# Performance work log

Hardware: AMD Instinct MI355X
Metric: run time of the kernel (lower is better)

Reference implementation:

```python
import jax, jax.numpy as jnp
import numpy as np

HID = 16

def _lrconv(x, edge_index, edge_attr, w1, b1, w2, b2):
    # flow='target_to_source': x_i = x[edge_index[0]], x_j = x[edge_index[1]],
    # aggregate (max) at edge_index[0].
    src = edge_index[0]
    dst = edge_index[1]
    m = jnp.concatenate([x[src], x[dst], edge_attr], axis=-1)  # [E, 2*in+edge]
    m = jax.nn.relu(m @ w1 + b1)
    m = jax.nn.relu(m @ w2 + b2)  # [E, out], all >= 0
    agg = jax.ops.segment_max(m, src, num_segments=x.shape[0])
    # empty segments get -inf in jax; PyG fills with 0. Messages are ReLU'd (>=0),
    # so clamping at 0 is exact.
    return jnp.maximum(agg, 0.0)

def _glorot(key, shape):
    fan_in, fan_out = shape
    lim = float(np.sqrt(6.0 / (fan_in + fan_out)))
    return jax.random.uniform(key, shape, jnp.float32, -lim, lim)

def setup_inputs() -> dict:
    key = jax.random.key(0)
    ks = jax.random.split(key, 16)
    N, E = 100000, 1600000
    x = jax.random.normal(ks[0], (N, 4), jnp.float32)
    edge_index = jax.random.randint(ks[1], (2, E), 0, N, jnp.int64)
    edge_attr = jax.random.normal(ks[2], (E, 8), jnp.float32)
    # conv1: in=4 -> cat dim 4*2+8=16
    c1_w1 = _glorot(ks[3], (16, HID)); c1_b1 = jnp.zeros((HID,), jnp.float32)
    c1_w2 = _glorot(ks[4], (HID, 16)); c1_b2 = jnp.zeros((16,), jnp.float32)
    # conv2: in=16 -> cat dim 16*2+8=40
    c2_w1 = _glorot(ks[5], (40, HID)); c2_b1 = jnp.zeros((HID,), jnp.float32)
    c2_w2 = _glorot(ks[6], (HID, 16)); c2_b2 = jnp.zeros((16,), jnp.float32)
    l1_w = _glorot(ks[7], (16, 16)); l1_b = jnp.zeros((16,), jnp.float32)
    l2_w = _glorot(ks[8], (16, 1)); l2_b = jnp.zeros((1,), jnp.float32)
    return {"x": x, "edge_index": edge_index, "edge_attr": edge_attr,
            "c1_w1": c1_w1, "c1_b1": c1_b1, "c1_w2": c1_w2, "c1_b2": c1_b2,
            "c2_w1": c2_w1, "c2_b1": c2_b1, "c2_w2": c2_w2, "c2_b2": c2_b2,
            "l1_w": l1_w, "l1_b": l1_b, "l2_w": l2_w, "l2_b": l2_b}

def reference(x, edge_index, edge_attr,
              c1_w1, c1_b1, c1_w2, c1_b2,
              c2_w1, c2_b1, c2_w2, c2_b2,
              l1_w, l1_b, l2_w, l2_b):
    h = _lrconv(x, edge_index, edge_attr, c1_w1, c1_b1, c1_w2, c1_b2)   # [N,16]
    h = _lrconv(h, edge_index, edge_attr, c2_w1, c2_b1, c2_w2, c2_b2)   # [N,16]
    h = jax.nn.relu(h @ l1_w + l1_b)
    return h @ l2_w + l2_b  # [N,1]
```

## Files before the change

### kernel.cpp

```cpp
#include <hip/hip_runtime.h>
#include <hip/hip_fp16.h>

#define CHUNK 1024
#define RECB 24
#define SPAN 192

typedef _Float16 half8 __attribute__((ext_vector_type(8)));
typedef _Float16 half4 __attribute__((ext_vector_type(4)));
typedef float floatx4 __attribute__((ext_vector_type(4)));

__device__ __forceinline__ unsigned int pack2f(float a, float b) {
    __half2 h = __floats2half2_rn(a, b);
    return *(unsigned int*)&h;
}

__device__ __forceinline__ half8 load_attr(const char* __restrict__ rec, int et) {
    union { unsigned int u[4]; half8 h; } cv;
    uint2 lo = *(const uint2*)(rec + (size_t)et * RECB + 8);
    uint2 hi = *(const uint2*)(rec + (size_t)et * RECB + 16);
    cv.u[0] = lo.x; cv.u[1] = lo.y; cv.u[2] = hi.x; cv.u[3] = hi.y;
    return cv.h;
}

__global__ __launch_bounds__(256) void rank_cvt(
    const int* __restrict__ ei, const float* __restrict__ x,
    int* __restrict__ deg, unsigned short* __restrict__ r,
    _Float16* __restrict__ xh, int E, int N)
{
    int e = blockIdx.x * 256 + threadIdx.x;
    if (e >= E) return;
    r[e] = (unsigned short)atomicAdd(&deg[ei[e]], 1);
    if (e < N) {
        float4 xv = *(const float4*)(x + (size_t)e * 4);
        half4 hx;
        hx[0] = (_Float16)xv.x; hx[1] = (_Float16)xv.y;
        hx[2] = (_Float16)xv.z; hx[3] = (_Float16)xv.w;
        *(half4*)(xh + (size_t)e * 4) = hx;
    }
}

__global__ __launch_bounds__(256) void scan_chunk_sums(
    const int* __restrict__ v, int* __restrict__ csum, int N)
{
    __shared__ int s[256];
    int base = blockIdx.x * CHUNK;
    int t = threadIdx.x;
    int acc = 0;
    #pragma unroll
    for (int i = 0; i < CHUNK / 256; ++i) {
        int idx = base + t + i * 256;
        if (idx < N) acc += v[idx];
    }
    s[t] = acc; __syncthreads();
    for (int o = 128; o > 0; o >>= 1) {
        if (t < o) s[t] += s[t + o];
        __syncthreads();
    }
    if (t == 0) csum[blockIdx.x] = s[0];
}

__global__ __launch_bounds__(256) void scan_chunk_off(
    const int* __restrict__ csum, int* __restrict__ coff, int nch)
{
    __shared__ int s[256];
    __shared__ int carry;
    int t = threadIdx.x;
    if (t == 0) carry = 0;
    __syncthreads();
    for (int base = 0; base < nch; base += 256) {
        int v = (base + t < nch) ? csum[base + t] : 0;
        s[t] = v; __syncthreads();
        for (int o = 1; o < 256; o <<= 1) {
            int add = (t >= o) ? s[t - o] : 0;
            __syncthreads();
            s[t] += add;
            __syncthreads();
        }
        int excl = carry + (t > 0 ? s[t - 1] : 0);
        if (base + t < nch) coff[base + t] = excl;
        __syncthreads();
        if (t == 0) carry += s[255];
        __syncthreads();
    }
}

__global__ __launch_bounds__(256) void scan_within_excl(
    const int* __restrict__ deg, int* __restrict__ pos,
    const int* __restrict__ coff, int N)
{
    __shared__ int s[256];
    int t = threadIdx.x;
    int base = blockIdx.x * CHUNK + t * 4;
    int v0 = 0, v1 = 0, v2 = 0, v3 = 0;
    if (base + 0 < N) v0 = deg[base + 0];
    if (base + 1 < N) v1 = deg[base + 1];
    if (base + 2 < N) v2 = deg[base + 2];
    if (base + 3 < N) v3 = deg[base + 3];
    s[t] = v0 + v1 + v2 + v3;
    __syncthreads();
    for (int o = 1; o < 256; o <<= 1) {
        int add = (t >= o) ? s[t - o] : 0;
        __syncthreads();
        s[t] += add;
        __syncthreads();
    }
    int run = coff[blockIdx.x] + (t > 0 ? s[t - 1] : 0);
    if (base + 0 < N) pos[base + 0] = run; run += v0;
    if (base + 1 < N) pos[base + 1] = run; run += v1;
    if (base + 2 < N) pos[base + 2] = run; run += v2;
    if (base + 3 < N) pos[base + 3] = run;
}

__global__ __launch_bounds__(256) void scatter_rec(
    const int* __restrict__ ei, const float* __restrict__ ea,
    const int* __restrict__ pos, const unsigned short* __restrict__ r,
    char* __restrict__ rec, int E)
{
    int e = blockIdx.x * 256 + threadIdx.x;
    if (e >= E) return;
    int s = ei[e];
    int d = ei[E + e];
    int p = pos[s] + (int)r[e];
    float4 a0 = *(const float4*)(ea + (size_t)e * 8);
    float4 a1 = *(const float4*)(ea + (size_t)e * 8 + 4);
    unsigned int h0 = pack2f(a0.x, a0.y), h1 = pack2f(a0.z, a0.w);
    unsigned int h2 = pack2f(a1.x, a1.y), h3 = pack2f(a1.z, a1.w);
    char* b = rec + (size_t)p * RECB;
    *(int2*)b         = make_int2(s, d);
    *(uint2*)(b + 8)  = make_uint2(h0, h1);
    *(uint2*)(b + 16) = make_uint2(h2, h3);
}

__global__ __launch_bounds__(256) void edge_mlp1_agg(
    const _Float16* __restrict__ xh,
    const char*  __restrict__ rec,
    const float* __restrict__ w1, const float* __restrict__ b1,
    const float* __restrict__ w2, const float* __restrict__ b2,
    int* __restrict__ aggi,
    int E)
{
    __shared__ _Float16 itm[4][8][16][24];
    __shared__ int lmax[SPAN * 16];
    int tid = threadIdx.x;
    int w = tid >> 6, lane = tid & 63;
    int e16 = lane & 15, q = lane >> 4;
    int kb = blockIdx.x * 512;
    int ebase = kb + (w << 7);
    int e0 = ebase + lane;
    int e1 = ebase + 64 + lane;

    #pragma unroll
    for (int i = 0; i < SPAN * 16 / 256; ++i) lmax[tid + i * 256] = 0;

    int klast = min(kb + 511, E - 1);
    int n_first = *(const int*)(rec + (size_t)kb * RECB);
    int n_last  = *(const int*)(rec + (size_t)klast * RECB);
    int span = n_last - n_first + 1;
    bool fb = (span > SPAN);
    __syncthreads();

    int s0 = 0, d0 = 0, s1 = 0, d1 = 0;
    if (e0 < E) { int2 p = *(const int2*)(rec + (size_t)e0 * RECB); s0 = p.x; d0 = p.y; }
    if (e1 < E) { int2 p = *(const int2*)(rec + (size_t)e1 * RECB); s1 = p.x; d1 = p.y; }

    half8 B1, B2;
    #pragma unroll
    for (int j = 0; j < 8; ++j) { B1[j] = (_Float16)0.f; B2[j] = (_Float16)0.f; }
    if (q < 2) {
        #pragma unroll
        for (int j = 0; j < 8; ++j) {
            B1[j] = (_Float16)w1[(8 * q + j) * 16 + e16];
            B2[j] = (_Float16)w2[(8 * q + j) * 16 + e16];
        }
    }
    float b1c = b1[e16], b2c = b2[e16];

    half8 A[8];
    #pragma unroll
    for (int t = 0; t < 8; ++t) {
        int tt = t & 3;
        int st = (t < 4) ? __shfl(s0, 16 * tt + e16, 64) : __shfl(s1, 16 * tt + e16, 64);
        int dt = (t < 4) ? __shfl(d0, 16 * tt + e16, 64) : __shfl(d1, 16 * tt + e16, 64);
        half8 a;
        #pragma unroll
        for (int j = 0; j < 8; ++j) a[j] = (_Float16)0.f;
        int et = ebase + 16 * t + e16;
        if (q == 0 && et < E) {
            half4 hs = *(const half4*)(xh + (size_t)st * 4);
            half4 hd = *(const half4*)(xh + (size_t)dt * 4);
            a[0] = hs[0]; a[1] = hs[1]; a[2] = hs[2]; a[3] = hs[3];
            a[4] = hd[0]; a[5] = hd[1]; a[6] = hd[2]; a[7] = hd[3];
        } else if (q == 1 && et < E) {
            a = load_attr(rec, et);
        }
        A[t] = a;
    }

    floatx4 C[8];
    #pragma unroll
    for (int t = 0; t < 8; ++t) {
        floatx4 c = {b1c, b1c, b1c, b1c};
        C[t] = __builtin_amdgcn_mfma_f32_16x16x32_f16(A[t], B1, c, 0, 0, 0);
    }
    #pragma unroll
    for (int t = 0; t < 8; ++t)
        #pragma unroll
        for (int i = 0; i < 4; ++i)
            itm[w][t][4 * q + i][e16] = (_Float16)fmaxf(C[t][i], 0.0f);
    __builtin_amdgcn_wave_barrier();

    half8 A2[8];
    #pragma unroll
    for (int t = 0; t < 8; ++t) {
        half8 a;
        #pragma unroll
        for (int j = 0; j < 8; ++j) a[j] = (_Float16)0.f;
        if (q < 2) a = *(const half8*)&itm[w][t][e16][8 * q];
        A2[t] = a;
    }
    __builtin_amdgcn_wave_barrier();
    floatx4 C2[8];
    #pragma unroll
    for (int t = 0; t < 8; ++t) {
        floatx4 c = {b2c, b2c, b2c, b2c};
        C2[t] = __builtin_amdgcn_mfma_f32_16x16x32_f16(A2[t], B2, c, 0, 0, 0);
    }

    #pragma unroll
    for (int t = 0; t < 8; ++t) {
        int tt = t & 3;
        #pragma unroll
        for (int i = 0; i < 4; ++i) {
            int rr = 4 * q + i;
            int nn = (t < 4) ? __shfl(s0, 16 * tt + rr, 64) : __shfl(s1, 16 * tt + rr, 64);
            int et = ebase + 16 * t + rr;
            if (et < E) {
                int bits = __float_as_int(fmaxf(C2[t][i], 0.0f));
                if (!fb) atomicMax(&lmax[(nn - n_first) * 16 + e16], bits);
                else     atomicMax(&aggi[(size_t)nn * 16 + e16], bits);
            }
        }
    }
    __syncthreads();
    if (!fb) {
        int tot = span * 16;
        for (int idx = tid; idx < tot; idx += 256) {
            int row = idx >> 4;
            int nn = n_first + row;
            int v = lmax[idx];
            if (nn == n_first || nn == n_last) {
                if (v != 0) atomicMax(&aggi[(size_t)nn * 16 + (idx & 15)], v);
            } else {
                aggi[(size_t)nn * 16 + (idx & 15)] = v;
            }
        }
    }
}

__global__ __launch_bounds__(256) void cvt_h1(
    const int* __restrict__ aggi, unsigned int* __restrict__ h1u, int total)
{
    int i = blockIdx.x * 256 + threadIdx.x;
    if (i >= total) return;
    int2 v = *(const int2*)(aggi + 2 * i);
    h1u[i] = pack2f(__int_as_float(v.x), __int_as_float(v.y));
}

__global__ __launch_bounds__(256) void edge_mlp2_agg(
    const _Float16* __restrict__ h1,
    const char*  __restrict__ rec,
    const float* __restrict__ w1, const float* __restrict__ b1v,
    const float* __restrict__ w2, const float* __restrict__ b2,
    int* __restrict__ aggi, int E)
{
    __shared__ _Float16 itm[4][8][16][24];
    __shared__ int lmax[SPAN * 16];
    int tid = threadIdx.x;
    int w = tid >> 6, lane = tid & 63;
    int e16 = lane & 15, q = lane >> 4;
    int kb = blockIdx.x * 512;
    int ebase = kb + (w << 7);
    int e0 = ebase + lane;
    int e1 = ebase + 64 + lane;

    #pragma unroll
    for (int i = 0; i < SPAN * 16 / 256; ++i) lmax[tid + i * 256] = 0;

    int klast = min(kb + 511, E - 1);
    int n_first = *(const int*)(rec + (size_t)kb * RECB);
    int n_last  = *(const int*)(rec + (size_t)klast * RECB);
    int span = n_last - n_first + 1;
    bool fb = (span > SPAN);
    __syncthreads();

    int s0 = 0, d0 = 0, s1 = 0, d1 = 0;
    if (e0 < E) { int2 p = *(const int2*)(rec + (size_t)e0 * RECB); s0 = p.x; d0 = p.y; }
    if (e1 < E) { int2 p = *(const int2*)(rec + (size_t)e1 * RECB); s1 = p.x; d1 = p.y; }

    half8 B1, B2e, BL2;
    #pragma unroll
    for (int j = 0; j < 8; ++j) {
        B1[j] = (_Float16)w1[(8 * q + j) * 16 + e16];
        B2e[j] = (_Float16)0.f; BL2[j] = (_Float16)0.f;
    }
    if (q == 0) {
        #pragma unroll
        for (int j = 0; j < 8; ++j)
            B2e[j] = (_Float16)w1[(32 + j) * 16 + e16];
    }
    if (q < 2) {
        #pragma unroll
        for (int j = 0; j < 8; ++j)
            BL2[j] = (_Float16)w2[(8 * q + j) * 16 + e16];
    }
    float b1c = b1v[e16], b2c = b2[e16];

    half8 A1[8];
    #pragma unroll
    for (int t = 0; t < 8; ++t) {
        int tt = t & 3;
        int st = (t < 4) ? __shfl(s0, 16 * tt + e16, 64) : __shfl(s1, 16 * tt + e16, 64);
        int dt = (t < 4) ? __shfl(d0, 16 * tt + e16, 64) : __shfl(d1, 16 * tt + e16, 64);
        int row = (q < 2) ? st : dt;
        A1[t] = *(const half8*)(h1 + (size_t)row * 16 + 8 * (q & 1));
    }

    floatx4 C[8];
    #pragma unroll
    for (int t = 0; t < 8; ++t) {
        half8 a2;
        #pragma unroll
        for (int j = 0; j < 8; ++j) a2[j] = (_Float16)0.f;
        int et = ebase + 16 * t + e16;
        if (q == 0 && et < E)
            a2 = load_attr(rec, et);
        floatx4 c = {b1c, b1c, b1c, b1c};
        c = __builtin_amdgcn_mfma_f32_16x16x32_f16(a2, B2e, c, 0, 0, 0);
        C[t] = __builtin_amdgcn_mfma_f32_16x16x32_f16(A1[t], B1, c, 0, 0, 0);
    }
    #pragma unroll
    for (int t = 0; t < 8; ++t)
        #pragma unroll
        for (int i = 0; i < 4; ++i)
            itm[w][t][4 * q + i][e16] = (_Float16)fmaxf(C[t][i], 0.0f);
    __builtin_amdgcn_wave_barrier();

    half8 A2L[8];
    #pragma unroll
    for (int t = 0; t < 8; ++t) {
        half8 a;
        #pragma unroll
        for (int j = 0; j < 8; ++j) a[j] = (_Float16)0.f;
        if (q < 2) a = *(const half8*)&itm[w][t][e16][8 * q];
        A2L[t] = a;
    }
    __builtin_amdgcn_wave_barrier();
    floatx4 C2[8];
    #pragma unroll
    for (int t = 0; t < 8; ++t) {
        floatx4 c = {b2c, b2c, b2c, b2c};
        C2[t] = __builtin_amdgcn_mfma_f32_16x16x32_f16(A2L[t], BL2, c, 0, 0, 0);
    }

    #pragma unroll
    for (int t = 0; t < 8; ++t) {
        int tt = t & 3;
        #pragma unroll
        for (int i = 0; i < 4; ++i) {
            int rr = 4 * q + i;
            int nn = (t < 4) ? __shfl(s0, 16 * tt + rr, 64) : __shfl(s1, 16 * tt + rr, 64);
            int et = ebase + 16 * t + rr;
            if (et < E) {
                int bits = __float_as_int(fmaxf(C2[t][i], 0.0f));
                if (!fb) atomicMax(&lmax[(nn - n_first) * 16 + e16], bits);
                else     atomicMax(&aggi[(size_t)nn * 16 + e16], bits);
            }
        }
    }
    __syncthreads();
    if (!fb) {
        int tot = span * 16;
        for (int idx = tid; idx < tot; idx += 256) {
            int row = idx >> 4;
            int nn = n_first + row;
            int v = lmax[idx];
            if (nn == n_first || nn == n_last) {
                if (v != 0) atomicMax(&aggi[(size_t)nn * 16 + (idx & 15)], v);
            } else {
                aggi[(size_t)nn * 16 + (idx & 15)] = v;
            }
        }
    }
}

__global__ __launch_bounds__(256) void head_out(
    const int* __restrict__ aggi,
    const float* __restrict__ l1w, const float* __restrict__ l1b,
    const float* __restrict__ l2w, const float* __restrict__ l2b,
    float* __restrict__ out, int N)
{
    int n = blockIdx.x * 256 + threadIdx.x;
    if (n >= N) return;
    const float4* ar = (const float4*)(aggi + (size_t)n * 16);
    float4 A0 = ar[0], A1 = ar[1], A2 = ar[2], A3 = ar[3];
    float acc[16] = {A0.x, A0.y, A0.z, A0.w, A1.x, A1.y, A1.z, A1.w,
                     A2.x, A2.y, A2.z, A2.w, A3.x, A3.y, A3.z, A3.w};
    float t2[16];
    #pragma unroll
    for (int j = 0; j < 16; ++j) t2[j] = l1b[j];
    #pragma unroll
    for (int k = 0; k < 16; ++k) {
        float ak = acc[k];
        #pragma unroll
        for (int j = 0; j < 16; ++j) t2[j] = fmaf(ak, l1w[k * 16 + j], t2[j]);
    }
    float r2 = l2b[0];
    #pragma unroll
    for (int j = 0; j < 16; ++j) r2 = fmaf(fmaxf(t2[j], 0.0f), l2w[j], r2);
    out[n] = r2;
}

extern "C" void kernel_launch(void* const* d_in, const int* in_sizes, int n_in,
                              void* d_out, int out_size, void* d_ws, size_t ws_size,
                              hipStream_t stream)
{
    const float* x     = (const float*)d_in[0];
    const int*   ei    = (const int*)  d_in[1];
    const float* ea    = (const float*)d_in[2];
    const float* c1_w1 = (const float*)d_in[3];
    const float* c1_b1 = (const float*)d_in[4];
    const float* c1_w2 = (const float*)d_in[5];
    const float* c1_b2 = (const float*)d_in[6];
    const float* c2_w1 = (const float*)d_in[7];
    const float* c2_b1 = (const float*)d_in[8];
    const float* c2_w2 = (const float*)d_in[9];
    const float* c2_b2 = (const float*)d_in[10];
    const float* l1_w  = (const float*)d_in[11];
    const float* l1_b  = (const float*)d_in[12];
    const float* l2_w  = (const float*)d_in[13];
    const float* l2_b  = (const float*)d_in[14];
    float* out = (float*)d_out;

    const int N = in_sizes[0] / 4;
    const int E = in_sizes[2] / 8;
    const int nch = (N + CHUNK - 1) / CHUNK;

    const int BLK = 256;
    const int egrid = (E + BLK - 1) / BLK;
    const int mgrid = (E + 511) / 512;
    const int ngrid = (N + 255) / 256;
    const int cgrid = (N * 8 + 255) / 256;

    size_t szPos = ((size_t)N * 4 + 255) & ~(size_t)255;
    size_t szR   = ((size_t)E * 2 + 255) & ~(size_t)255;
    size_t szXh  = ((size_t)N * 8 + 255) & ~(size_t)255;
    size_t szH1  = ((size_t)N * 32 + 255) & ~(size_t)255;
    size_t szRec = ((size_t)E * RECB + 255) & ~(size_t)255;
    size_t szAgg = ((size_t)N * 16 * 4 + 255) & ~(size_t)255;
    size_t szDeg = szPos;

    size_t pos_off  = 0;
    size_t r_off    = pos_off  + szPos;
    size_t xh_off   = r_off    + szR;
    size_t h1_off   = xh_off   + szXh;
    size_t rec_off  = h1_off   + szH1;
    size_t agg1_off = rec_off  + szRec;
    size_t agg2_off = agg1_off + szAgg;
    size_t deg_off  = agg2_off + szAgg;
    size_t cs_off   = deg_off  + szDeg;
    size_t cf_off   = cs_off   + 4096;

    int*            pos  = (int*)  ((char*)d_ws + pos_off);
    unsigned short* r    = (unsigned short*)((char*)d_ws + r_off);
    _Float16*       xh   = (_Float16*)((char*)d_ws + xh_off);
    _Float16*       h1   = (_Float16*)((char*)d_ws + h1_off);
    char*           rec  = (char*) ((char*)d_ws + rec_off);
    int*            agg1 = (int*)  ((char*)d_ws + agg1_off);
    int*            agg2 = (int*)  ((char*)d_ws + agg2_off);
    int*            deg  = (int*)  ((char*)d_ws + deg_off);
    int*            csum = (int*)  ((char*)d_ws + cs_off);
    int*            coff = (int*)  ((char*)d_ws + cf_off);

    hipMemsetAsync(deg, 0, (size_t)N * 4, stream);
    hipMemsetAsync(agg1, 0, (size_t)N * 64, stream);
    hipMemsetAsync(agg2, 0, (size_t)N * 64, stream);
    rank_cvt<<<egrid, BLK, 0, stream>>>(ei, x, deg, r, xh, E, N);
    scan_chunk_sums<<<nch, BLK, 0, stream>>>(deg, csum, N);
    scan_chunk_off<<<1, 256, 0, stream>>>(csum, coff, nch);
    scan_within_excl<<<nch, BLK, 0, stream>>>(deg, pos, coff, N);
    scatter_rec<<<egrid, BLK, 0, stream>>>(ei, ea, pos, r, rec, E);
    edge_mlp1_agg<<<mgrid, BLK, 0, stream>>>(xh, rec,
                                             c1_w1, c1_b1, c1_w2, c1_b2,
                                             agg1, E);
    cvt_h1<<<cgrid, BLK, 0, stream>>>(agg1, (unsigned int*)h1, N * 8);
    edge_mlp2_agg<<<mgrid, BLK, 0, stream>>>(h1, rec,
                                             c2_w1, c2_b1, c2_w2, c2_b2,
                                             agg2, E);
    head_out<<<ngrid, BLK, 0, stream>>>(agg2, l1_w, l1_b, l2_w, l2_b, out, N);
}
```

Baseline: 324.9 us.

## Replace global-atomic counting sort with two-pass bucketed partition into split SoA arrays

The per-edge global atomic rank plus random 24-byte record scatter is replaced by a two-level counting sort. Per-block shared-memory histograms over 512-node buckets are scanned, edges are partitioned into buckets, then each bucket is sorted by source in shared memory. Records are split into an int2 src/dst array and a 16-byte attribute array, so the MLP kernels use aligned vector loads. This trades global atomic contention and scattered writes for an extra full pass over the edge data, and reuses the partition buffers for the aggregation arrays.

```diff
diff --git a/kernel.cpp b/kernel.cpp
--- a/kernel.cpp
+++ b/kernel.cpp
@@ -2,7 +2,8 @@
 #include <hip/hip_fp16.h>
 
 #define CHUNK 1024
-#define RECB 24
+#define NBLK 256
+#define NSH  9
 #define SPAN 192
 
 typedef _Float16 half8 __attribute__((ext_vector_type(8)));
@@ -14,29 +15,35 @@
     return *(unsigned int*)&h;
 }
 
-__device__ __forceinline__ half8 load_attr(const char* __restrict__ rec, int et) {
-    union { unsigned int u[4]; half8 h; } cv;
-    uint2 lo = *(const uint2*)(rec + (size_t)et * RECB + 8);
-    uint2 hi = *(const uint2*)(rec + (size_t)et * RECB + 16);
-    cv.u[0] = lo.x; cv.u[1] = lo.y; cv.u[2] = hi.x; cv.u[3] = hi.y;
+__device__ __forceinline__ half8 load_attr(const uint4* __restrict__ rat, int et) {
+    union { uint4 u; half8 h; } cv;
+    cv.u = rat[et];
     return cv.h;
 }
 
-__global__ __launch_bounds__(256) void rank_cvt(
+__global__ __launch_bounds__(512) void hist_x(
     const int* __restrict__ ei, const float* __restrict__ x,
-    int* __restrict__ deg, unsigned short* __restrict__ r,
-    _Float16* __restrict__ xh, int E, int N)
-{
-    int e = blockIdx.x * 256 + threadIdx.x;
-    if (e >= E) return;
-    r[e] = (unsigned short)atomicAdd(&deg[ei[e]], 1);
-    if (e < N) {
-        float4 xv = *(const float4*)(x + (size_t)e * 4);
-        half4 hx;
-        hx[0] = (_Float16)xv.x; hx[1] = (_Float16)xv.y;
-        hx[2] = (_Float16)xv.z; hx[3] = (_Float16)xv.w;
-        *(half4*)(xh + (size_t)e * 4) = hx;
-    }
+    int* __restrict__ cnt, _Float16* __restrict__ xh,
+    int E, int N, int nbk, int epb)
+{
+    __shared__ int h[256];
+    int t = threadIdx.x, b = blockIdx.x;
+    if (t < 256) h[t] = 0;
+    __syncthreads();
+    int est = b * epb;
+    int een = min(E, est + epb);
+    for (int e = est + t; e < een; e += 512)
+        atomicAdd(&h[ei[e] >> NSH], 1);
+    for (int i = est + t; i < een; i += 512)
+        if (i < N) {
+            float4 xv = *(const float4*)(x + (size_t)i * 4);
+            half4 hx;
+            hx[0] = (_Float16)xv.x; hx[1] = (_Float16)xv.y;
+            hx[2] = (_Float16)xv.z; hx[3] = (_Float16)xv.w;
+            *(half4*)(xh + (size_t)i * 4) = hx;
+        }
+    __syncthreads();
+    if (t < nbk) cnt[t * NBLK + b] = h[t];
 }
 
 __global__ __launch_bounds__(256) void scan_chunk_sums(
@@ -111,29 +118,69 @@
     if (base + 3 < N) pos[base + 3] = run;
 }
 
-__global__ __launch_bounds__(256) void scatter_rec(
+__global__ __launch_bounds__(512) void partition(
     const int* __restrict__ ei, const float* __restrict__ ea,
-    const int* __restrict__ pos, const unsigned short* __restrict__ r,
-    char* __restrict__ rec, int E)
-{
-    int e = blockIdx.x * 256 + threadIdx.x;
-    if (e >= E) return;
-    int s = ei[e];
-    int d = ei[E + e];
-    int p = pos[s] + (int)r[e];
-    float4 a0 = *(const float4*)(ea + (size_t)e * 8);
-    float4 a1 = *(const float4*)(ea + (size_t)e * 8 + 4);
-    unsigned int h0 = pack2f(a0.x, a0.y), h1 = pack2f(a0.z, a0.w);
-    unsigned int h2 = pack2f(a1.x, a1.y), h3 = pack2f(a1.z, a1.w);
-    char* b = rec + (size_t)p * RECB;
-    *(int2*)b         = make_int2(s, d);
-    *(uint2*)(b + 8)  = make_uint2(h0, h1);
-    *(uint2*)(b + 16) = make_uint2(h2, h3);
+    const int* __restrict__ off,
+    int2* __restrict__ p1sd, uint4* __restrict__ p1at,
+    int E, int nbk, int epb)
+{
+    __shared__ int cur[256];
+    int t = threadIdx.x, b = blockIdx.x;
+    if (t < nbk) cur[t] = off[t * NBLK + b];
+    __syncthreads();
+    int est = b * epb;
+    int een = min(E, est + epb);
+    for (int e = est + t; e < een; e += 512) {
+        int s = ei[e], d = ei[E + e];
+        float4 a0 = *(const float4*)(ea + (size_t)e * 8);
+        float4 a1 = *(const float4*)(ea + (size_t)e * 8 + 4);
+        uint4 at;
+        at.x = pack2f(a0.x, a0.y); at.y = pack2f(a0.z, a0.w);
+        at.z = pack2f(a1.x, a1.y); at.w = pack2f(a1.z, a1.w);
+        int p = atomicAdd(&cur[s >> NSH], 1);
+        p1sd[p] = make_int2(s, d);
+        p1at[p] = at;
+    }
+}
+
+__global__ __launch_bounds__(512) void bucket_csr(
+    const int2* __restrict__ p1sd, const uint4* __restrict__ p1at,
+    const int* __restrict__ off,
+    int2* __restrict__ rsd, uint4* __restrict__ rat,
+    int E, int nbk)
+{
+    __shared__ int h[512];
+    __shared__ int cur[512];
+    int t = threadIdx.x, k = blockIdx.x;
+    int base = off[k * NBLK];
+    int end = (k + 1 < nbk) ? off[(k + 1) * NBLK] : E;
+    int n0 = k << NSH;
+    h[t] = 0;
+    __syncthreads();
+    for (int p = base + t; p < end; p += 512)
+        atomicAdd(&h[p1sd[p].x - n0], 1);
+    __syncthreads();
+    for (int o = 1; o < 512; o <<= 1) {
+        int v = (t >= o) ? h[t - o] : 0;
+        __syncthreads();
+        h[t] += v;
+        __syncthreads();
+    }
+    cur[t] = base + (t ? h[t - 1] : 0);
+    __syncthreads();
+    for (int p = base + t; p < end; p += 512) {
+        int2 sd = p1sd[p];
+        uint4 at = p1at[p];
+        int q = atomicAdd(&cur[sd.x - n0], 1);
+        rsd[q] = sd;
+        rat[q] = at;
+    }
 }
 
 __global__ __launch_bounds__(256) void edge_mlp1_agg(
     const _Float16* __restrict__ xh,
-    const char*  __restrict__ rec,
+    const int2*  __restrict__ rsd,
+    const uint4* __restrict__ rat,
     const float* __restrict__ w1, const float* __restrict__ b1,
     const float* __restrict__ w2, const float* __restrict__ b2,
     int* __restrict__ aggi,
@@ -153,15 +200,15 @@
     for (int i = 0; i < SPAN * 16 / 256; ++i) lmax[tid + i * 256] = 0;
 
     int klast = min(kb + 511, E - 1);
-    int n_first = *(const int*)(rec + (size_t)kb * RECB);
-    int n_last  = *(const int*)(rec + (size_t)klast * RECB);
+    int n_first = rsd[kb].x;
+    int n_last  = rsd[klast].x;
     int span = n_last - n_first + 1;
     bool fb = (span > SPAN);
     __syncthreads();
 
     int s0 = 0, d0 = 0, s1 = 0, d1 = 0;
-    if (e0 < E) { int2 p = *(const int2*)(rec + (size_t)e0 * RECB); s0 = p.x; d0 = p.y; }
-    if (e1 < E) { int2 p = *(const int2*)(rec + (size_t)e1 * RECB); s1 = p.x; d1 = p.y; }
+    if (e0 < E) { int2 p = rsd[e0]; s0 = p.x; d0 = p.y; }
+    if (e1 < E) { int2 p = rsd[e1]; s1 = p.x; d1 = p.y; }
 
     half8 B1, B2;
     #pragma unroll
@@ -191,7 +238,7 @@
             a[0] = hs[0]; a[1] = hs[1]; a[2] = hs[2]; a[3] = hs[3];
             a[4] = hd[0]; a[5] = hd[1]; a[6] = hd[2]; a[7] = hd[3];
         } else if (q == 1 && et < E) {
-            a = load_attr(rec, et);
+            a = load_attr(rat, et);
         }
         A[t] = a;
     }
@@ -268,7 +315,8 @@
 
 __global__ __launch_bounds__(256) void edge_mlp2_agg(
     const _Float16* __restrict__ h1,
-    const char*  __restrict__ rec,
+    const int2*  __restrict__ rsd,
+    const uint4* __restrict__ rat,
     const float* __restrict__ w1, const float* __restrict__ b1v,
     const float* __restrict__ w2, const float* __restrict__ b2,
     int* __restrict__ aggi, int E)
@@ -287,15 +335,15 @@
     for (int i = 0; i < SPAN * 16 / 256; ++i) lmax[tid + i * 256] = 0;
 
     int klast = min(kb + 511, E - 1);
-    int n_first = *(const int*)(rec + (size_t)kb * RECB);
-    int n_last  = *(const int*)(rec + (size_t)klast * RECB);
+    int n_first = rsd[kb].x;
+    int n_last  = rsd[klast].x;
     int span = n_last - n_first + 1;
     bool fb = (span > SPAN);
     __syncthreads();
 
     int s0 = 0, d0 = 0, s1 = 0, d1 = 0;
-    if (e0 < E) { int2 p = *(const int2*)(rec + (size_t)e0 * RECB); s0 = p.x; d0 = p.y; }
-    if (e1 < E) { int2 p = *(const int2*)(rec + (size_t)e1 * RECB); s1 = p.x; d1 = p.y; }
+    if (e0 < E) { int2 p = rsd[e0]; s0 = p.x; d0 = p.y; }
+    if (e1 < E) { int2 p = rsd[e1]; s1 = p.x; d1 = p.y; }
 
     half8 B1, B2e, BL2;
     #pragma unroll
@@ -333,7 +381,7 @@
         for (int j = 0; j < 8; ++j) a2[j] = (_Float16)0.f;
         int et = ebase + 16 * t + e16;
         if (q == 0 && et < E)
-            a2 = load_attr(rec, et);
+            a2 = load_attr(rat, et);
         floatx4 c = {b1c, b1c, b1c, b1c};
         c = __builtin_amdgcn_mfma_f32_16x16x32_f16(a2, B2e, c, 0, 0, 0);
         C[t] = __builtin_amdgcn_mfma_f32_16x16x32_f16(A1[t], B1, c, 0, 0, 0);
@@ -443,57 +491,62 @@
 
     const int N = in_sizes[0] / 4;
     const int E = in_sizes[2] / 8;
-    const int nch = (N + CHUNK - 1) / CHUNK;
+    const int nbk = (N + (1 << NSH) - 1) >> NSH;
+    const int epb = (E + NBLK - 1) / NBLK;
+    const int ntot = nbk * NBLK;
+    const int nch = (ntot + CHUNK - 1) / CHUNK;
 
     const int BLK = 256;
-    const int egrid = (E + BLK - 1) / BLK;
     const int mgrid = (E + 511) / 512;
     const int ngrid = (N + 255) / 256;
     const int cgrid = (N * 8 + 255) / 256;
 
-    size_t szPos = ((size_t)N * 4 + 255) & ~(size_t)255;
-    size_t szR   = ((size_t)E * 2 + 255) & ~(size_t)255;
     size_t szXh  = ((size_t)N * 8 + 255) & ~(size_t)255;
     size_t szH1  = ((size_t)N * 32 + 255) & ~(size_t)255;
-    size_t szRec = ((size_t)E * RECB + 255) & ~(size_t)255;
-    size_t szAgg = ((size_t)N * 16 * 4 + 255) & ~(size_t)255;
-    size_t szDeg = szPos;
-
-    size_t pos_off  = 0;
-    size_t r_off    = pos_off  + szPos;
-    size_t xh_off   = r_off    + szR;
+    size_t szSd  = ((size_t)E * 8 + 255) & ~(size_t)255;
+    size_t szAt  = ((size_t)E * 16 + 255) & ~(size_t)255;
+    size_t szCnt = ((size_t)ntot * 4 + 255) & ~(size_t)255;
+    size_t szAgg = ((size_t)N * 64 + 255) & ~(size_t)255;
+
+    size_t xh_off   = 0;
     size_t h1_off   = xh_off   + szXh;
-    size_t rec_off  = h1_off   + szH1;
-    size_t agg1_off = rec_off  + szRec;
-    size_t agg2_off = agg1_off + szAgg;
-    size_t deg_off  = agg2_off + szAgg;
-    size_t cs_off   = deg_off  + szDeg;
+    size_t rsd_off  = h1_off   + szH1;
+    size_t rat_off  = rsd_off  + szSd;
+    size_t p1sd_off = rat_off  + szAt;
+    size_t p1at_off = p1sd_off + szSd;
+    size_t cnt_off  = p1at_off + szAt;
+    size_t off_off  = cnt_off  + szCnt;
+    size_t cs_off   = off_off  + szCnt;
     size_t cf_off   = cs_off   + 4096;
-
-    int*            pos  = (int*)  ((char*)d_ws + pos_off);
-    unsigned short* r    = (unsigned short*)((char*)d_ws + r_off);
-    _Float16*       xh   = (_Float16*)((char*)d_ws + xh_off);
-    _Float16*       h1   = (_Float16*)((char*)d_ws + h1_off);
-    char*           rec  = (char*) ((char*)d_ws + rec_off);
-    int*            agg1 = (int*)  ((char*)d_ws + agg1_off);
-    int*            agg2 = (int*)  ((char*)d_ws + agg2_off);
-    int*            deg  = (int*)  ((char*)d_ws + deg_off);
-    int*            csum = (int*)  ((char*)d_ws + cs_off);
-    int*            coff = (int*)  ((char*)d_ws + cf_off);
-
-    hipMemsetAsync(deg, 0, (size_t)N * 4, stream);
+    size_t agg1_off = p1sd_off;
+    size_t agg2_off = p1sd_off + szAgg;
+
+    _Float16* xh   = (_Float16*)((char*)d_ws + xh_off);
+    _Float16* h1   = (_Float16*)((char*)d_ws + h1_off);
+    int2*     rsd  = (int2*)    ((char*)d_ws + rsd_off);
+    uint4*    rat  = (uint4*)   ((char*)d_ws + rat_off);
+    int2*     p1sd = (int2*)    ((char*)d_ws + p1sd_off);
+    uint4*    p1at = (uint4*)   ((char*)d_ws + p1at_off);
+    int*      cnt  = (int*)     ((char*)d_ws + cnt_off);
+    int*      off  = (int*)     ((char*)d_ws + off_off);
+    int*      csum = (int*)     ((char*)d_ws + cs_off);
+    int*      coff = (int*)     ((char*)d_ws + cf_off);
+    int*      agg1 = (int*)     ((char*)d_ws + agg1_off);
+    int*      agg2 = (int*)     ((char*)d_ws + agg2_off);
+
+    hist_x<<<NBLK, 512, 0, stream>>>(ei, x, cnt, xh, E, N, nbk, epb);
+    scan_chunk_sums<<<nch, BLK, 0, stream>>>(cnt, csum, ntot);
+    scan_chunk_off<<<1, 256, 0, stream>>>(csum, coff, nch);
+    scan_within_excl<<<nch, BLK, 0, stream>>>(cnt, off, coff, ntot);
+    partition<<<NBLK, 512, 0, stream>>>(ei, ea, off, p1sd, p1at, E, nbk, epb);
+    bucket_csr<<<nbk, 512, 0, stream>>>(p1sd, p1at, off, rsd, rat, E, nbk);
     hipMemsetAsync(agg1, 0, (size_t)N * 64, stream);
     hipMemsetAsync(agg2, 0, (size_t)N * 64, stream);
-    rank_cvt<<<egrid, BLK, 0, stream>>>(ei, x, deg, r, xh, E, N);
-    scan_chunk_sums<<<nch, BLK, 0, stream>>>(deg, csum, N);
-    scan_chunk_off<<<1, 256, 0, stream>>>(csum, coff, nch);
-    scan_within_excl<<<nch, BLK, 0, stream>>>(deg, pos, coff, N);
-    scatter_rec<<<egrid, BLK, 0, stream>>>(ei, ea, pos, r, rec, E);
-    edge_mlp1_agg<<<mgrid, BLK, 0, stream>>>(xh, rec,
+    edge_mlp1_agg<<<mgrid, BLK, 0, stream>>>(xh, rsd, rat,
                                              c1_w1, c1_b1, c1_w2, c1_b2,
                                              agg1, E);
     cvt_h1<<<cgrid, BLK, 0, stream>>>(agg1, (unsigned int*)h1, N * 8);
-    edge_mlp2_agg<<<mgrid, BLK, 0, stream>>>(h1, rec,
+    edge_mlp2_agg<<<mgrid, BLK, 0, stream>>>(h1, rsd, rat,
                                              c2_w1, c2_b1, c2_w2, c2_b2,
                                              agg2, E);
     head_out<<<ngrid, BLK, 0, stream>>>(agg2, l1_w, l1_b, l2_w, l2_b, out, N);
```

After: 303.7 us. -6.6%, faster.
